# Performance work log

Measured on AMD Instinct MI355X. Metric: run time of the kernel, lower is better.

Reference implementation:

```python
import jax, jax.numpy as jnp
import numpy as np
import math

H, KVH, DH = 8, 1, 256
CAP = 50.0
THETA = 10000.0
HIDDEN = [2048, 1024, 1024]


def _rope_cos_sin(pos, dh=DH, theta=THETA):
    # pos: [b, s] int -> cos/sin: [b, s, dh] (Gemma style: freqs duplicated)
    inv_freq = 1.0 / (theta ** (jnp.arange(0, dh, 2, dtype=jnp.float32) / dh))
    freqs = pos.astype(jnp.float32)[..., None] * inv_freq  # [b, s, dh/2]
    emb = jnp.concatenate([freqs, freqs], axis=-1)
    return jnp.cos(emb), jnp.sin(emb)


def _rotate_half(x):
    x1, x2 = jnp.split(x, 2, axis=-1)
    return jnp.concatenate([-x2, x1], axis=-1)


def _apply_rope(q, k, cos, sin):
    # q: [b,H,s,d], k: [b,KVH,s,d]; cos/sin: [b,s,d] -> broadcast over heads
    c = cos[:, None].astype(q.dtype)
    s = sin[:, None].astype(q.dtype)
    return q * c + _rotate_half(q) * s, k * c + _rotate_half(k) * s


def setup_inputs() -> dict:
    key = jax.random.key(0)
    ks = jax.random.split(key, 32)
    inp = {
        'hs0': jax.random.normal(ks[0], (8, 968, 2048), jnp.float32),
        'hs1': jax.random.normal(ks[1], (8, 6, 1024), jnp.float32),
        'hs2': jax.random.normal(ks[2], (8, 50, 1024), jnp.float32),
        'attention_mask': jnp.zeros((8, 1, 1024, 1024), jnp.float32),
        'pos0': jnp.sort(jax.random.randint(ks[3], (8, 968), 0, 1024), axis=-1),
        'pos1': jnp.sort(jax.random.randint(ks[4], (8, 6), 0, 1024), axis=-1),
        'pos2': jnp.sort(jax.random.randint(ks[5], (8, 50), 0, 1024), axis=-1),
    }
    ki = 6
    for b, hid in enumerate(HIDDEN):
        inp[f'wq{b}'] = 0.02 * jax.random.normal(ks[ki + 0], (hid, H * DH), jnp.float32)
        inp[f'wk{b}'] = 0.02 * jax.random.normal(ks[ki + 1], (hid, KVH * DH), jnp.float32)
        inp[f'wv{b}'] = 0.02 * jax.random.normal(ks[ki + 2], (hid, KVH * DH), jnp.float32)
        inp[f'wo{b}'] = 0.02 * jax.random.normal(ks[ki + 3], (H * DH, hid), jnp.float32)
        ki += 4
    return inp


def _joint_attn(hs_all, pos_all, mask, wq, wk, wv, wo):
    b = hs_all[0].shape[0]
    q_lens = [h.shape[1] for h in hs_all]
    qs, kss, vs = [], [], []
    for hs, pos, Wq, Wk, Wv in zip(hs_all, pos_all, wq, wk, wv):
        s = hs.shape[1]
        q = (hs @ Wq).reshape(b, s, H, DH).transpose(0, 2, 1, 3)
        k = (hs @ Wk).reshape(b, s, KVH, DH).transpose(0, 2, 1, 3)
        v = (hs @ Wv).reshape(b, s, KVH, DH).transpose(0, 2, 1, 3)
        cos, sin = _rope_cos_sin(pos)
        q, k = _apply_rope(q, k, cos, sin)
        # repeat_kv: MQA -> expand KV heads to H
        qs.append(q)
        kss.append(jnp.repeat(k, H // KVH, axis=1))
        vs.append(jnp.repeat(v, H // KVH, axis=1))
    q = jnp.concatenate(qs, axis=2)   # [b,H,S,d]
    k = jnp.concatenate(kss, axis=2)
    v = jnp.concatenate(vs, axis=2)
    scores = jnp.einsum('bhqd,bhkd->bhqk', q, k) / math.sqrt(DH)
    scores = jnp.tanh(scores / CAP) * CAP + mask  # tanh soft-capping
    p = jax.nn.softmax(scores.astype(jnp.float32), axis=-1).astype(q.dtype)
    out = jnp.einsum('bhqk,bhkd->bhqd', p, v)     # [b,H,S,d]
    out = out.transpose(0, 2, 1, 3).reshape(b, sum(q_lens), H * DH)
    outs, off = [], 0
    for ql, Wo in zip(q_lens, wo):
        outs.append(out[:, off:off + ql] @ Wo)
        off += ql
    return tuple(outs)


def reference(hs0, hs1, hs2, attention_mask, pos0, pos1, pos2,
              wq0, wk0, wv0, wo0, wq1, wk1, wv1, wo1, wq2, wk2, wv2, wo2):
    return _joint_attn((hs0, hs1, hs2), (pos0, pos1, pos2), attention_mask,
                       (wq0, wq1, wq2), (wk0, wk1, wk2), (wv0, wv1, wv2),
                       (wo0, wo1, wo2))
```

## Files before the change

kernel.cpp:

```cpp
#include <hip/hip_runtime.h>
#include <hip/hip_bf16.h>
#include <math.h>

namespace {
constexpr int Bn = 8, Sn = 1024, Hn = 8, DHn = 256, HDn = 2048;
constexpr size_t QB0 = 0;
constexpr size_t QB1 = (size_t)20 * 64 * 4096;
constexpr size_t QB2 = QB1 + (size_t)20 * 32 * 4096;
constexpr size_t HB0 = 0;
constexpr size_t HB1 = (size_t)61 * 64 * 4096;
constexpr size_t HB2 = HB1 + (size_t)1 * 32 * 4096;
constexpr size_t OB0 = 0;
constexpr size_t OB1 = (size_t)16 * 64 * 4096;
constexpr size_t OB2 = OB1 + (size_t)8 * 64 * 4096;
}

using bf16x8 = __attribute__((ext_vector_type(8))) short;
using f32x4  = __attribute__((ext_vector_type(4))) float;

__device__ __forceinline__ float bf2f(unsigned short u) {
  unsigned int x = ((unsigned int)u) << 16;
  return __builtin_bit_cast(float, x);
}
__device__ __forceinline__ unsigned short f2bf(float f) {
  unsigned int x = __builtin_bit_cast(unsigned int, f);
  x += 0x7fff + ((x >> 16) & 1);
  return (unsigned short)(x >> 16);
}
__device__ __forceinline__ bf16x8 pack8(const float4& u, const float4& v) {
  bf16x8 r;
  r[0] = (short)f2bf(u.x); r[1] = (short)f2bf(u.y); r[2] = (short)f2bf(u.z); r[3] = (short)f2bf(u.w);
  r[4] = (short)f2bf(v.x); r[5] = (short)f2bf(v.y); r[6] = (short)f2bf(v.z); r[7] = (short)f2bf(v.w);
  return r;
}
__device__ __forceinline__ void gload_lds16(const void* g, void* l) {
  __builtin_amdgcn_global_load_lds(
      (const __attribute__((address_space(1))) void*)g,
      (__attribute__((address_space(3))) void*)l, 16, 0, 0);
}

__device__ __forceinline__ void convW_body(
    const float* __restrict__ W, unsigned short* __restrict__ dstBase,
    int K, int N, int nb, int kb, float (*S)[132], int t)
{
  const int kl = t >> 5, nq = (t & 31) * 4;
  for (int kk = kl; kk < 64; kk += 8) {
    const float4 v = *(const float4*)(W + (size_t)(kb * 64 + kk) * N + nb * 128 + nq);
    S[kk][nq] = v.x; S[kk][nq + 1] = v.y; S[kk][nq + 2] = v.z; S[kk][nq + 3] = v.w;
  }
  __syncthreads();
  unsigned short* chunk = dstBase + ((size_t)nb * (K >> 5) + kb * 2) * 4096;
#pragma unroll
  for (int j = 0; j < 4; ++j) {
    const int q = t * 4 + j;
    const int r = q >> 3, g = q & 7;
    bf16x8 o;
#pragma unroll
    for (int e = 0; e < 8; ++e) o[e] = (short)f2bf(S[g * 8 + e][r]);
    *(bf16x8*)(chunk + (g >> 2) * 4096 + r * 32 + (((g & 3) ^ ((r >> 1) & 3)) * 8)) = o;
  }
}

__global__ __launch_bounds__(256) void convAll(
    const float* __restrict__ wq0, const float* __restrict__ wk0, const float* __restrict__ wv0,
    const float* __restrict__ wq1, const float* __restrict__ wk1, const float* __restrict__ wv1,
    const float* __restrict__ wq2, const float* __restrict__ wk2, const float* __restrict__ wv2,
    const float* __restrict__ hs0, const float* __restrict__ hs1, const float* __restrict__ hs2,
    unsigned short* __restrict__ qkvT, unsigned short* __restrict__ hsT)
{
  __shared__ float S[64][132];
  const int bid = blockIdx.x;
  const int t = threadIdx.x;

  if (bid < 1280) {
    const float* W; unsigned short* dst; int K, N, nb, kb;
    if (bid < 512)       { W = wq0; dst = qkvT + QB0;                  K = 2048; N = 2048; nb = bid & 15; kb = bid >> 4; }
    else if (bid < 576)  { int r = bid - 512;  W = wk0; dst = qkvT + QB0 + (size_t)16 * 64 * 4096; K = 2048; N = 256; nb = r & 1; kb = r >> 1; }
    else if (bid < 640)  { int r = bid - 576;  W = wv0; dst = qkvT + QB0 + (size_t)18 * 64 * 4096; K = 2048; N = 256; nb = r & 1; kb = r >> 1; }
    else if (bid < 896)  { int r = bid - 640;  W = wq1; dst = qkvT + QB1;                  K = 1024; N = 2048; nb = r & 15; kb = r >> 4; }
    else if (bid < 928)  { int r = bid - 896;  W = wk1; dst = qkvT + QB1 + (size_t)16 * 32 * 4096; K = 1024; N = 256; nb = r & 1; kb = r >> 1; }
    else if (bid < 960)  { int r = bid - 928;  W = wv1; dst = qkvT + QB1 + (size_t)18 * 32 * 4096; K = 1024; N = 256; nb = r & 1; kb = r >> 1; }
    else if (bid < 1216) { int r = bid - 960;  W = wq2; dst = qkvT + QB2;                  K = 1024; N = 2048; nb = r & 15; kb = r >> 4; }
    else if (bid < 1248) { int r = bid - 1216; W = wk2; dst = qkvT + QB2 + (size_t)16 * 32 * 4096; K = 1024; N = 256; nb = r & 1; kb = r >> 1; }
    else                 { int r = bid - 1248; W = wv2; dst = qkvT + QB2 + (size_t)18 * 32 * 4096; K = 1024; N = 256; nb = r & 1; kb = r >> 1; }
    convW_body(W, dst, K, N, nb, kb, S, t);
  } else {
    const float* A; unsigned short* dst; int K, M_total, mb, kb;
    if (bid < 3232)      { int it = bid - 1280; A = hs0; dst = hsT + HB0; K = 2048; M_total = 7744; mb = it >> 5; kb = it & 31; }
    else if (bid < 3248) { int it = bid - 3232; A = hs1; dst = hsT + HB1; K = 1024; M_total = 48;   mb = 0;       kb = it; }
    else                 { int it = bid - 3248; A = hs2; dst = hsT + HB2; K = 1024; M_total = 400;  mb = it >> 4; kb = it & 15; }
    unsigned short* chunk = dst + ((size_t)mb * (K >> 5) + kb * 2) * 4096;
#pragma unroll
    for (int j = 0; j < 4; ++j) {
      const int q = j * 256 + t;
      const int r = q >> 3, g = q & 7;
      int m = mb * 128 + r;
      if (m >= M_total) m = mb * 128;
      const float* src = A + (size_t)m * K + kb * 64 + g * 8;
      const float4 u = *(const float4*)(src);
      const float4 v = *(const float4*)(src + 4);
      *(bf16x8*)(chunk + (g >> 2) * 4096 + r * 32 + (((g & 3) ^ ((r >> 1) & 3)) * 8)) = pack8(u, v);
    }
  }
}

__global__ __launch_bounds__(256) void convWo(
    const float* __restrict__ wo0, const float* __restrict__ wo1, const float* __restrict__ wo2,
    unsigned short* __restrict__ woT)
{
  __shared__ float S[64][132];
  const int bid = blockIdx.x;
  const float* W; unsigned short* dst; int N, nb, kb;
  if (bid < 512)      { W = wo0; dst = woT + OB0; N = 2048; nb = bid & 15; kb = bid >> 4; }
  else if (bid < 768) { int r = bid - 512; W = wo1; dst = woT + OB1; N = 1024; nb = r & 7; kb = r >> 3; }
  else                { int r = bid - 768; W = wo2; dst = woT + OB2; N = 1024; nb = r & 7; kb = r >> 3; }
  convW_body(W, dst, HDn, N, nb, kb, S, threadIdx.x);
}

__global__ __launch_bounds__(256) void gemm_qkv(
    const unsigned short* __restrict__ hsT, const unsigned short* __restrict__ qkvT,
    unsigned short* __restrict__ Qh, unsigned short* __restrict__ Kh,
    unsigned short* __restrict__ Vt)
{
  __shared__ __align__(16) short As[2][4096];
  __shared__ __align__(16) short Bs[2][4096];
  const int tid = threadIdx.x;
  const int w  = tid >> 6, l = tid & 63;
  const int wm = w >> 1,  wn = w & 1;
  const int lc = l & 15,  lg = l >> 4;

  const int bid = blockIdx.x;
  int bx, by, L, K, c_off, M_total;
  const unsigned short *aBase, *wBase;
  if (bid < 1220)      { bx = bid % 20; by = bid / 20; L = 968; K = 2048; c_off = 0;   M_total = 7744; aBase = hsT + HB0; wBase = qkvT + QB0; }
  else if (bid < 1240) { bx = bid - 1220; by = 0;      L = 6;   K = 1024; c_off = 968; M_total = 48;   aBase = hsT + HB1; wBase = qkvT + QB1; }
  else                 { int r = bid - 1240; bx = r % 20; by = r / 20; L = 50; K = 1024; c_off = 974; M_total = 400; aBase = hsT + HB2; wBase = qkvT + QB2; }
  const int kcN = K >> 5;
  const int bm0 = by * 128;

  int region, nbL, cb0;
  if (bx < 16)      { region = 0; nbL = bx;      cb0 = bx * 128; }
  else if (bx < 18) { region = 1; nbL = bx - 16; cb0 = (bx - 16) * 128; }
  else              { region = 2; nbL = bx - 18; cb0 = (bx - 18) * 128; }
  const unsigned short* WTr = wBase +
      (region == 0 ? (size_t)0 : (region == 1 ? (size_t)16 * kcN * 4096
                                              : (size_t)18 * kcN * 4096));
  const char* bChunk0 = (const char*)(WTr + (size_t)nbL * kcN * 4096);
  const char* aChunk0 = (const char*)(aBase + (size_t)by * kcN * 4096);

  f32x4 acc[4][4];
#pragma unroll
  for (int i = 0; i < 4; ++i)
#pragma unroll
    for (int j = 0; j < 4; ++j) acc[i][j] = (f32x4){0.f, 0.f, 0.f, 0.f};

  auto issue = [&](int kc, int nb) {
    const char* sa = aChunk0 + (size_t)kc * 8192;
    const char* sb = bChunk0 + (size_t)kc * 8192;
    char* da = (char*)&As[nb][0];
    char* db = (char*)&Bs[nb][0];
    gload_lds16(sa + tid * 16, da + tid * 16);
    gload_lds16(sa + tid * 16 + 4096, da + tid * 16 + 4096);
    gload_lds16(sb + tid * 16, db + tid * 16);
    gload_lds16(sb + tid * 16 + 4096, db + tid * 16 + 4096);
  };

  issue(0, 0);
  for (int kt = 0; kt < kcN; ++kt) {
    const int cur = kt & 1;
    __builtin_amdgcn_s_barrier();
    if (kt + 1 < kcN) {
      issue(kt + 1, cur ^ 1);
      asm volatile("s_waitcnt vmcnt(4)" ::: "memory");
    } else {
      asm volatile("s_waitcnt vmcnt(0)" ::: "memory");
    }
    __builtin_amdgcn_s_barrier();
    __builtin_amdgcn_sched_barrier(0);
    bf16x8 af[4], bfg[4];
#pragma unroll
    for (int mi = 0; mi < 4; ++mi) {
      const int row = wm * 64 + mi * 16 + lc;
      af[mi] = *(const bf16x8*)((const char*)&As[cur][0] + row * 64 +
                                ((lg ^ ((row >> 1) & 3)) * 16));
    }
#pragma unroll
    for (int ni = 0; ni < 4; ++ni) {
      const int row = wn * 64 + ni * 16 + lc;
      bfg[ni] = *(const bf16x8*)((const char*)&Bs[cur][0] + row * 64 +
                                 ((lg ^ ((row >> 1) & 3)) * 16));
    }
#pragma unroll
    for (int mi = 0; mi < 4; ++mi)
#pragma unroll
      for (int ni = 0; ni < 4; ++ni)
        acc[mi][ni] = __builtin_amdgcn_mfma_f32_16x16x32_bf16(af[mi], bfg[ni], acc[mi][ni], 0, 0, 0);
  }

#pragma unroll
  for (int mi = 0; mi < 4; ++mi) {
    const int gm = bm0 + wm * 64 + mi * 16 + lg * 4;
#pragma unroll
    for (int r = 0; r < 4; ++r) {
      const int m = gm + r;
      if (m < M_total) {
        const int cb = m / L, cs = m - cb * L;
#pragma unroll
        for (int ni = 0; ni < 4; ++ni) {
          const int colL = cb0 + wn * 64 + ni * 16 + lc;
          const unsigned short v = f2bf(acc[mi][ni][r]);
          if (region == 0) {
            const int hh = colL >> 8, dd = colL & 255;
            Qh[(((size_t)cb * Hn + hh) * Sn + c_off + cs) * DHn + dd] = v;
          } else if (region == 1) {
            Kh[((size_t)cb * Sn + c_off + cs) * DHn + colL] = v;
          } else {
            Vt[((size_t)cb * DHn + colL) * Sn + c_off + cs] = v;
          }
        }
      }
    }
  }
}

__global__ __launch_bounds__(256) void gemm_wo(
    const unsigned short* __restrict__ A, const unsigned short* __restrict__ woT,
    float* __restrict__ C)
{
  __shared__ __align__(16) short As[2][4096];
  __shared__ __align__(16) short Bs[2][4096];
  const int tid = threadIdx.x;
  const int w  = tid >> 6, l = tid & 63;
  const int wm = w >> 1,  wn = w & 1;
  const int lc = l & 15,  lg = l >> 4;

  const int bid = blockIdx.x;
  int bx, by, L, N, a_off, M_total;
  const unsigned short* wb;
  float* Cg;
  if (bid < 976)      { bx = bid & 15; by = bid >> 4; L = 968; N = 2048; a_off = 0;   M_total = 7744; wb = woT + OB0; Cg = C; }
  else if (bid < 984) { bx = bid - 976; by = 0;       L = 6;   N = 1024; a_off = 968; M_total = 48;   wb = woT + OB1; Cg = C + (size_t)7744 * 2048; }
  else                { int r = bid - 984; bx = r & 7; by = r >> 3; L = 50; N = 1024; a_off = 974; M_total = 400; wb = woT + OB2; Cg = C + (size_t)7744 * 2048 + (size_t)48 * 1024; }
  const int bm0 = by * 128;
  const char* chunk0 = (const char*)(wb + (size_t)bx * 64 * 4096);

  const int gcont = (tid & 3) ^ ((tid >> 3) & 3);
  const char* aRow[2];
#pragma unroll
  for (int j = 0; j < 2; ++j) {
    int m = bm0 + (tid >> 2) + j * 64;
    if (m >= M_total) m = 0;
    const int cb = m / L, cs = m - cb * L;
    aRow[j] = (const char*)(A + (size_t)(cb * Sn + a_off + cs) * HDn) + gcont * 16;
  }

  f32x4 acc[4][4];
#pragma unroll
  for (int i = 0; i < 4; ++i)
#pragma unroll
    for (int j = 0; j < 4; ++j) acc[i][j] = (f32x4){0.f, 0.f, 0.f, 0.f};

  auto issue = [&](int kc, int nb) {
    char* da = (char*)&As[nb][0];
    char* db = (char*)&Bs[nb][0];
    gload_lds16(aRow[0] + (size_t)kc * 64, da + tid * 16);
    gload_lds16(aRow[1] + (size_t)kc * 64, da + tid * 16 + 4096);
    const char* sb = chunk0 + (size_t)kc * 8192;
    gload_lds16(sb + tid * 16, db + tid * 16);
    gload_lds16(sb + tid * 16 + 4096, db + tid * 16 + 4096);
  };

  issue(0, 0);
  for (int kt = 0; kt < 64; ++kt) {
    const int cur = kt & 1;
    __builtin_amdgcn_s_barrier();
    if (kt + 1 < 64) {
      issue(kt + 1, cur ^ 1);
      asm volatile("s_waitcnt vmcnt(4)" ::: "memory");
    } else {
      asm volatile("s_waitcnt vmcnt(0)" ::: "memory");
    }
    __builtin_amdgcn_s_barrier();
    __builtin_amdgcn_sched_barrier(0);
    bf16x8 af[4], bfg[4];
#pragma unroll
    for (int mi = 0; mi < 4; ++mi) {
      const int row = wm * 64 + mi * 16 + lc;
      af[mi] = *(const bf16x8*)((const char*)&As[cur][0] + row * 64 +
                                ((lg ^ ((row >> 1) & 3)) * 16));
    }
#pragma unroll
    for (int ni = 0; ni < 4; ++ni) {
      const int row = wn * 64 + ni * 16 + lc;
      bfg[ni] = *(const bf16x8*)((const char*)&Bs[cur][0] + row * 64 +
                                 ((lg ^ ((row >> 1) & 3)) * 16));
    }
#pragma unroll
    for (int mi = 0; mi < 4; ++mi)
#pragma unroll
      for (int ni = 0; ni < 4; ++ni)
        acc[mi][ni] = __builtin_amdgcn_mfma_f32_16x16x32_bf16(af[mi], bfg[ni], acc[mi][ni], 0, 0, 0);
  }

#pragma unroll
  for (int mi = 0; mi < 4; ++mi) {
    const int gm = bm0 + wm * 64 + mi * 16 + lg * 4;
#pragma unroll
    for (int r = 0; r < 4; ++r) {
      const int m = gm + r;
      if (m < M_total) {
        const int cb = m / L, cs = m - cb * L;
#pragma unroll
        for (int ni = 0; ni < 4; ++ni) {
          const int col = bx * 128 + wn * 64 + ni * 16 + lc;
          Cg[(size_t)(cb * L + cs) * N + col] = acc[mi][ni][r];
        }
      }
    }
  }
}

__global__ __launch_bounds__(128) void rope_k(
    unsigned short* __restrict__ Kh,
    const int* __restrict__ p0, const int* __restrict__ p1, const int* __restrict__ p2)
{
  const int t = blockIdx.x, b = t >> 10, s = t & 1023;
  int p;
  if (s < 968)      p = p0[b * 968 + s];
  else if (s < 974) p = p1[b * 6 + (s - 968)];
  else              p = p2[b * 50 + (s - 974)];
  const float pf = (float)p;
  const float c0 = -0.07195578415606394f;
  const int d = threadIdx.x;
  const float inv = __expf(c0 * (float)d);
  float cs, sn;
  sincosf(pf * inv, &sn, &cs);
  unsigned short* base = Kh + ((size_t)b * Sn + s) * DHn;
  const float x1 = bf2f(base[d]), x2 = bf2f(base[d + 128]);
  base[d]       = f2bf(x1 * cs - x2 * sn);
  base[d + 128] = f2bf(x2 * cs + x1 * sn);
}

__global__ __launch_bounds__(512) void attn_mfma(
    const unsigned short* __restrict__ Qh, const unsigned short* __restrict__ Kh,
    const unsigned short* __restrict__ Vt, const float* __restrict__ mask,
    const int* __restrict__ p0, const int* __restrict__ p1, const int* __restrict__ p2,
    unsigned short* __restrict__ O)
{
  __shared__ __align__(16) short KsB[2][8192];
  __shared__ __align__(16) short VsB[2][8192];
  __shared__ __align__(16) float Ms[2][512];
  __shared__ __align__(16) short Pb[8][512];
  const int tid = threadIdx.x;
  const int w  = tid >> 6;
  const int l  = tid & 63;
  const int lc = l & 15;
  const int lg = l >> 4;
  const int q0 = blockIdx.x * 16;
  const int b  = blockIdx.z;
  const int srow = q0 + lc;

  const char* KgB = (const char*)(Kh + (size_t)b * Sn * DHn);
  const char* VgB = (const char*)(Vt + (size_t)b * DHn * Sn);

  auto stage = [&](int kt, int nb) {
    const char* kg = KgB + (size_t)kt * 16384;
    const char* vg = VgB + (size_t)kt * 64;
#pragma unroll
    for (int j = 0; j < 2; ++j) {
      const int chunk = w * 2 + j;
      const int o = chunk * 1024 + l * 16;
      const int srcK = o ^ (((o >> 9) & 7) << 4);
      gload_lds16(kg + srcK, (char*)&KsB[nb][0] + chunk * 1024);
    }
#pragma unroll
    for (int j = 0; j < 2; ++j) {
      const int chunk = w * 2 + j;
      const int o = chunk * 1024 + l * 16;
      const int x = o ^ (((o >> 7) & 3) << 4);
      gload_lds16(vg + (size_t)(x >> 6) * 2048 + (x & 63),
                  (char*)&VsB[nb][0] + chunk * 1024);
    }
    if (l < 16) {
      const float* mg = mask + ((size_t)b * Sn + q0 + 2 * w + (l >> 3)) * Sn
                             + kt * 32 + (l & 7) * 4;
      gload_lds16(mg, (char*)&Ms[nb][0] + w * 256);
    }
  };

  stage(0, 0);

  int p;
  if (srow < 968)      p = p0[b * 968 + srow];
  else if (srow < 974) p = p1[b * 6 + (srow - 968)];
  else                 p = p2[b * 50 + (srow - 974)];
  const float pf = (float)p;
  const float c0 = -0.07195578415606394f;

  const unsigned short* qrow = Qh + (((size_t)b * Hn + w) * Sn + srow) * DHn;
  bf16x8 qf[8];
#pragma unroll
  for (int dt = 0; dt < 8; ++dt)
    qf[dt] = *(const bf16x8*)(qrow + dt * 32 + lg * 8);
#pragma unroll
  for (int dt = 0; dt < 4; ++dt) {
#pragma unroll
    for (int j = 0; j < 8; ++j) {
      const int d = dt * 32 + lg * 8 + j;
      const float inv = __expf(c0 * (float)d);
      float cs, sn;
      sincosf(pf * inv, &sn, &cs);
      const float x1 = bf2f((unsigned short)qf[dt][j]);
      const float x2 = bf2f((unsigned short)qf[dt + 4][j]);
      qf[dt][j]     = (short)f2bf(x1 * cs - x2 * sn);
      qf[dt + 4][j] = (short)f2bf(x2 * cs + x1 * sn);
    }
  }

  f32x4 accO[16];
#pragma unroll
  for (int i = 0; i < 16; ++i) accO[i] = (f32x4){0.f, 0.f, 0.f, 0.f};
  float lsum[4] = {0.f, 0.f, 0.f, 0.f};

  const float C1 = 3.6067376022e-3f;
  const float RC = -144.26950408889634f;
  const float L2E = 1.4426950408889634f;

  int cur = 0;
  for (int kt = 0; kt < 32; ++kt) {
    if (kt + 1 < 32) {
      stage(kt + 1, cur ^ 1);
      asm volatile("s_waitcnt vmcnt(5)" ::: "memory");
    } else {
      asm volatile("s_waitcnt vmcnt(0)" ::: "memory");
    }
    __builtin_amdgcn_s_barrier();
    __builtin_amdgcn_sched_barrier(0);

    const short* Ks = &KsB[cur][0];
    const short* Vs = &VsB[cur][0];
    const float* Mw = &Ms[cur][0];

    f32x4 sc[2];
    __builtin_amdgcn_s_setprio(1);
#pragma unroll
    for (int ct = 0; ct < 2; ++ct) {
      f32x4 acc = (f32x4){0.f, 0.f, 0.f, 0.f};
      const int row = ct * 16 + lc;
      const int sw = (row & 7) << 4;
#pragma unroll
      for (int dt = 0; dt < 8; ++dt) {
        const int byt = (row * 512 + dt * 64 + lg * 16) ^ sw;
        const bf16x8 kf = *(const bf16x8*)((const char*)Ks + byt);
        acc = __builtin_amdgcn_mfma_f32_16x16x32_bf16(qf[dt], kf, acc, 0, 0, 0);
      }
      sc[ct] = acc;
    }
    __builtin_amdgcn_s_setprio(0);

#pragma unroll
    for (int ct = 0; ct < 2; ++ct) {
#pragma unroll
      for (int r = 0; r < 4; ++r) {
        const int row_p = lg * 4 + r;
        const float mv = Mw[row_p * 32 + ct * 16 + lc];
        const float e2 = __builtin_amdgcn_exp2f(sc[ct][r] * C1);
        const float rr = __builtin_amdgcn_rcpf(e2 + 1.f);
        const float pv = __builtin_amdgcn_exp2f(fmaf(rr, RC, mv * L2E));
        lsum[r] += pv;
        const int col = ct * 16 + lc;
        const int gp = (col >> 3) ^ ((row_p >> 1) & 3);
        *((short*)((char*)&Pb[w][0] + row_p * 64 + gp * 16 + (col & 7) * 2)) =
            (short)f2bf(pv);
      }
    }
    const int gp2 = lg ^ ((lc >> 1) & 3);
    const bf16x8 pfr = *(const bf16x8*)((const char*)&Pb[w][0] + lc * 64 + gp2 * 16);

    __builtin_amdgcn_s_setprio(1);
#pragma unroll
    for (int nt = 0; nt < 16; ++nt) {
      const int row = nt * 16 + lc;
      const int byt = (row * 64 + lg * 16) ^ (((row >> 1) & 3) << 4);
      const bf16x8 vf = *(const bf16x8*)((const char*)Vs + byt);
      accO[nt] = __builtin_amdgcn_mfma_f32_16x16x32_bf16(pfr, vf, accO[nt], 0, 0, 0);
    }
    __builtin_amdgcn_s_setprio(0);

    __builtin_amdgcn_s_barrier();
    cur ^= 1;
  }

#pragma unroll
  for (int mm = 1; mm < 16; mm <<= 1) {
#pragma unroll
    for (int r = 0; r < 4; ++r) lsum[r] += __shfl_xor(lsum[r], mm);
  }
  float rinv[4];
#pragma unroll
  for (int r = 0; r < 4; ++r) rinv[r] = 1.f / lsum[r];

  unsigned short* obase = O + ((size_t)b * Sn + q0 + lg * 4) * HDn + w * DHn + lc;
#pragma unroll
  for (int nt = 0; nt < 16; ++nt)
#pragma unroll
    for (int r = 0; r < 4; ++r)
      obase[(size_t)r * HDn + nt * 16] = f2bf(accO[nt][r] * rinv[r]);
}

extern "C" void kernel_launch(void* const* d_in, const int* in_sizes, int n_in,
                              void* d_out, int out_size, void* d_ws, size_t ws_size,
                              hipStream_t stream) {
  (void)in_sizes; (void)n_in; (void)out_size; (void)ws_size;
  const float* hs0  = (const float*)d_in[0];
  const float* hs1  = (const float*)d_in[1];
  const float* hs2  = (const float*)d_in[2];
  const float* mask = (const float*)d_in[3];
  const int*   pos0 = (const int*)d_in[4];
  const int*   pos1 = (const int*)d_in[5];
  const int*   pos2 = (const int*)d_in[6];
  float* out = (float*)d_out;

  unsigned short* Qh = (unsigned short*)d_ws;
  unsigned short* Kh = Qh + (size_t)Bn * Sn * HDn;
  unsigned short* Vt = Kh + (size_t)Bn * Sn * DHn;
  unsigned short* Ob = Vt + (size_t)Bn * Sn * DHn;
  unsigned short* qkvT = Ob;
  unsigned short* woT  = Qh;
  unsigned short* hsT  = (unsigned short*)out;

  hipLaunchKernelGGL(convAll, dim3(3312), dim3(256), 0, stream,
                     (const float*)d_in[7],  (const float*)d_in[8],  (const float*)d_in[9],
                     (const float*)d_in[11], (const float*)d_in[12], (const float*)d_in[13],
                     (const float*)d_in[15], (const float*)d_in[16], (const float*)d_in[17],
                     hs0, hs1, hs2, qkvT, hsT);

  hipLaunchKernelGGL(gemm_qkv, dim3(1320), dim3(256), 0, stream,
                     hsT, qkvT, Qh, Kh, Vt);

  hipLaunchKernelGGL(rope_k, dim3(Bn * Sn), dim3(128), 0, stream, Kh, pos0, pos1, pos2);
  hipLaunchKernelGGL(attn_mfma, dim3(Sn / 16, 1, Bn), dim3(512), 0, stream,
                     Qh, Kh, Vt, mask, pos0, pos1, pos2, Ob);

  hipLaunchKernelGGL(convWo, dim3(1024), dim3(256), 0, stream,
                     (const float*)d_in[10], (const float*)d_in[14], (const float*)d_in[18], woT);

  hipLaunchKernelGGL(gemm_wo, dim3(1016), dim3(256), 0, stream, Ob, woT, out);
}
```

Before: 424.7 us.

## Process two heads per wave in attention to reuse K/V fragment loads

```diff
diff --git a/kernel.cpp b/kernel.cpp
--- a/kernel.cpp
+++ b/kernel.cpp
@@ -341,7 +341,7 @@
   base[d + 128] = f2bf(x2 * cs + x1 * sn);
 }
 
-__global__ __launch_bounds__(512) void attn_mfma(
+__global__ __launch_bounds__(256) void attn_mfma(
     const unsigned short* __restrict__ Qh, const unsigned short* __restrict__ Kh,
     const unsigned short* __restrict__ Vt, const float* __restrict__ mask,
     const int* __restrict__ p0, const int* __restrict__ p1, const int* __restrict__ p2,
@@ -350,7 +350,7 @@
   __shared__ __align__(16) short KsB[2][8192];
   __shared__ __align__(16) short VsB[2][8192];
   __shared__ __align__(16) float Ms[2][512];
-  __shared__ __align__(16) short Pb[8][512];
+  __shared__ __align__(16) short Pb[4][1024];
   const int tid = threadIdx.x;
   const int w  = tid >> 6;
   const int l  = tid & 63;
@@ -367,24 +367,24 @@
     const char* kg = KgB + (size_t)kt * 16384;
     const char* vg = VgB + (size_t)kt * 64;
 #pragma unroll
-    for (int j = 0; j < 2; ++j) {
-      const int chunk = w * 2 + j;
+    for (int j = 0; j < 4; ++j) {
+      const int chunk = w * 4 + j;
       const int o = chunk * 1024 + l * 16;
       const int srcK = o ^ (((o >> 9) & 7) << 4);
       gload_lds16(kg + srcK, (char*)&KsB[nb][0] + chunk * 1024);
     }
 #pragma unroll
-    for (int j = 0; j < 2; ++j) {
-      const int chunk = w * 2 + j;
+    for (int j = 0; j < 4; ++j) {
+      const int chunk = w * 4 + j;
       const int o = chunk * 1024 + l * 16;
       const int x = o ^ (((o >> 7) & 3) << 4);
       gload_lds16(vg + (size_t)(x >> 6) * 2048 + (x & 63),
                   (char*)&VsB[nb][0] + chunk * 1024);
     }
-    if (l < 16) {
-      const float* mg = mask + ((size_t)b * Sn + q0 + 2 * w + (l >> 3)) * Sn
+    if (l < 32) {
+      const float* mg = mask + ((size_t)b * Sn + q0 + 4 * w + (l >> 3)) * Sn
                              + kt * 32 + (l & 7) * 4;
-      gload_lds16(mg, (char*)&Ms[nb][0] + w * 256);
+      gload_lds16(mg, (char*)&Ms[nb][0] + w * 512);
     }
   };
 
@@ -397,11 +397,14 @@
   const float pf = (float)p;
   const float c0 = -0.07195578415606394f;
 
-  const unsigned short* qrow = Qh + (((size_t)b * Hn + w) * Sn + srow) * DHn;
-  bf16x8 qf[8];
-#pragma unroll
-  for (int dt = 0; dt < 8; ++dt)
-    qf[dt] = *(const bf16x8*)(qrow + dt * 32 + lg * 8);
+  const unsigned short* qrowA = Qh + (((size_t)b * Hn + 2 * w) * Sn + srow) * DHn;
+  const unsigned short* qrowB = Qh + (((size_t)b * Hn + 2 * w + 1) * Sn + srow) * DHn;
+  bf16x8 qfA[8], qfB[8];
+#pragma unroll
+  for (int dt = 0; dt < 8; ++dt) {
+    qfA[dt] = *(const bf16x8*)(qrowA + dt * 32 + lg * 8);
+    qfB[dt] = *(const bf16x8*)(qrowB + dt * 32 + lg * 8);
+  }
 #pragma unroll
   for (int dt = 0; dt < 4; ++dt) {
 #pragma unroll
@@ -410,17 +413,29 @@
       const float inv = __expf(c0 * (float)d);
       float cs, sn;
       sincosf(pf * inv, &sn, &cs);
-      const float x1 = bf2f((unsigned short)qf[dt][j]);
-      const float x2 = bf2f((unsigned short)qf[dt + 4][j]);
-      qf[dt][j]     = (short)f2bf(x1 * cs - x2 * sn);
-      qf[dt + 4][j] = (short)f2bf(x2 * cs + x1 * sn);
-    }
-  }
-
-  f32x4 accO[16];
-#pragma unroll
-  for (int i = 0; i < 16; ++i) accO[i] = (f32x4){0.f, 0.f, 0.f, 0.f};
-  float lsum[4] = {0.f, 0.f, 0.f, 0.f};
+      {
+        const float x1 = bf2f((unsigned short)qfA[dt][j]);
+        const float x2 = bf2f((unsigned short)qfA[dt + 4][j]);
+        qfA[dt][j]     = (short)f2bf(x1 * cs - x2 * sn);
+        qfA[dt + 4][j] = (short)f2bf(x2 * cs + x1 * sn);
+      }
+      {
+        const float x1 = bf2f((unsigned short)qfB[dt][j]);
+        const float x2 = bf2f((unsigned short)qfB[dt + 4][j]);
+        qfB[dt][j]     = (short)f2bf(x1 * cs - x2 * sn);
+        qfB[dt + 4][j] = (short)f2bf(x2 * cs + x1 * sn);
+      }
+    }
+  }
+
+  f32x4 accA[16], accB[16];
+#pragma unroll
+  for (int i = 0; i < 16; ++i) {
+    accA[i] = (f32x4){0.f, 0.f, 0.f, 0.f};
+    accB[i] = (f32x4){0.f, 0.f, 0.f, 0.f};
+  }
+  float lsumA[4] = {0.f, 0.f, 0.f, 0.f};
+  float lsumB[4] = {0.f, 0.f, 0.f, 0.f};
 
   const float C1 = 3.6067376022e-3f;
   const float RC = -144.26950408889634f;
@@ -430,7 +445,7 @@
   for (int kt = 0; kt < 32; ++kt) {
     if (kt + 1 < 32) {
       stage(kt + 1, cur ^ 1);
-      asm volatile("s_waitcnt vmcnt(5)" ::: "memory");
+      asm volatile("s_waitcnt vmcnt(9)" ::: "memory");
     } else {
       asm volatile("s_waitcnt vmcnt(0)" ::: "memory");
     }
@@ -441,20 +456,22 @@
     const short* Vs = &VsB[cur][0];
     const float* Mw = &Ms[cur][0];
 
-    f32x4 sc[2];
+    f32x4 scA[2], scB[2];
     __builtin_amdgcn_s_setprio(1);
 #pragma unroll
     for (int ct = 0; ct < 2; ++ct) {
-      f32x4 acc = (f32x4){0.f, 0.f, 0.f, 0.f};
+      f32x4 aA = (f32x4){0.f, 0.f, 0.f, 0.f};
+      f32x4 aB = (f32x4){0.f, 0.f, 0.f, 0.f};
       const int row = ct * 16 + lc;
       const int sw = (row & 7) << 4;
 #pragma unroll
       for (int dt = 0; dt < 8; ++dt) {
         const int byt = (row * 512 + dt * 64 + lg * 16) ^ sw;
         const bf16x8 kf = *(const bf16x8*)((const char*)Ks + byt);
-        acc = __builtin_amdgcn_mfma_f32_16x16x32_bf16(qf[dt], kf, acc, 0, 0, 0);
+        aA = __builtin_amdgcn_mfma_f32_16x16x32_bf16(qfA[dt], kf, aA, 0, 0, 0);
+        aB = __builtin_amdgcn_mfma_f32_16x16x32_bf16(qfB[dt], kf, aB, 0, 0, 0);
       }
-      sc[ct] = acc;
+      scA[ct] = aA; scB[ct] = aB;
     }
     __builtin_amdgcn_s_setprio(0);
 
@@ -463,19 +480,29 @@
 #pragma unroll
       for (int r = 0; r < 4; ++r) {
         const int row_p = lg * 4 + r;
-        const float mv = Mw[row_p * 32 + ct * 16 + lc];
-        const float e2 = __builtin_amdgcn_exp2f(sc[ct][r] * C1);
-        const float rr = __builtin_amdgcn_rcpf(e2 + 1.f);
-        const float pv = __builtin_amdgcn_exp2f(fmaf(rr, RC, mv * L2E));
-        lsum[r] += pv;
         const int col = ct * 16 + lc;
+        const float mvl = Mw[row_p * 32 + col] * L2E;
         const int gp = (col >> 3) ^ ((row_p >> 1) & 3);
-        *((short*)((char*)&Pb[w][0] + row_p * 64 + gp * 16 + (col & 7) * 2)) =
-            (short)f2bf(pv);
+        const int pbyt = row_p * 64 + gp * 16 + (col & 7) * 2;
+        {
+          const float e2 = __builtin_amdgcn_exp2f(scA[ct][r] * C1);
+          const float rr = __builtin_amdgcn_rcpf(e2 + 1.f);
+          const float pv = __builtin_amdgcn_exp2f(fmaf(rr, RC, mvl));
+          lsumA[r] += pv;
+          *((short*)((char*)&Pb[w][0] + pbyt)) = (short)f2bf(pv);
+        }
+        {
+          const float e2 = __builtin_amdgcn_exp2f(scB[ct][r] * C1);
+          const float rr = __builtin_amdgcn_rcpf(e2 + 1.f);
+          const float pv = __builtin_amdgcn_exp2f(fmaf(rr, RC, mvl));
+          lsumB[r] += pv;
+          *((short*)((char*)&Pb[w][0] + 1024 + pbyt)) = (short)f2bf(pv);
+        }
       }
     }
     const int gp2 = lg ^ ((lc >> 1) & 3);
-    const bf16x8 pfr = *(const bf16x8*)((const char*)&Pb[w][0] + lc * 64 + gp2 * 16);
+    const bf16x8 pfA = *(const bf16x8*)((const char*)&Pb[w][0] + lc * 64 + gp2 * 16);
+    const bf16x8 pfB = *(const bf16x8*)((const char*)&Pb[w][0] + 1024 + lc * 64 + gp2 * 16);
 
     __builtin_amdgcn_s_setprio(1);
 #pragma unroll
@@ -483,7 +510,8 @@
       const int row = nt * 16 + lc;
       const int byt = (row * 64 + lg * 16) ^ (((row >> 1) & 3) << 4);
       const bf16x8 vf = *(const bf16x8*)((const char*)Vs + byt);
-      accO[nt] = __builtin_amdgcn_mfma_f32_16x16x32_bf16(pfr, vf, accO[nt], 0, 0, 0);
+      accA[nt] = __builtin_amdgcn_mfma_f32_16x16x32_bf16(pfA, vf, accA[nt], 0, 0, 0);
+      accB[nt] = __builtin_amdgcn_mfma_f32_16x16x32_bf16(pfB, vf, accB[nt], 0, 0, 0);
     }
     __builtin_amdgcn_s_setprio(0);
 
@@ -494,18 +522,27 @@
 #pragma unroll
   for (int mm = 1; mm < 16; mm <<= 1) {
 #pragma unroll
-    for (int r = 0; r < 4; ++r) lsum[r] += __shfl_xor(lsum[r], mm);
-  }
-  float rinv[4];
-#pragma unroll
-  for (int r = 0; r < 4; ++r) rinv[r] = 1.f / lsum[r];
-
-  unsigned short* obase = O + ((size_t)b * Sn + q0 + lg * 4) * HDn + w * DHn + lc;
+    for (int r = 0; r < 4; ++r) {
+      lsumA[r] += __shfl_xor(lsumA[r], mm);
+      lsumB[r] += __shfl_xor(lsumB[r], mm);
+    }
+  }
+  float rinvA[4], rinvB[4];
+#pragma unroll
+  for (int r = 0; r < 4; ++r) {
+    rinvA[r] = 1.f / lsumA[r];
+    rinvB[r] = 1.f / lsumB[r];
+  }
+
+  unsigned short* obA = O + ((size_t)b * Sn + q0 + lg * 4) * HDn + (2 * w) * DHn + lc;
+  unsigned short* obB = obA + DHn;
 #pragma unroll
   for (int nt = 0; nt < 16; ++nt)
 #pragma unroll
-    for (int r = 0; r < 4; ++r)
-      obase[(size_t)r * HDn + nt * 16] = f2bf(accO[nt][r] * rinv[r]);
+    for (int r = 0; r < 4; ++r) {
+      obA[(size_t)r * HDn + nt * 16] = f2bf(accA[nt][r] * rinvA[r]);
+      obB[(size_t)r * HDn + nt * 16] = f2bf(accB[nt][r] * rinvB[r]);
+    }
 }
 
 extern "C" void kernel_launch(void* const* d_in, const int* in_sizes, int n_in,
@@ -539,7 +576,7 @@
                      hsT, qkvT, Qh, Kh, Vt);
 
   hipLaunchKernelGGL(rope_k, dim3(Bn * Sn), dim3(128), 0, stream, Kh, pos0, pos1, pos2);
-  hipLaunchKernelGGL(attn_mfma, dim3(Sn / 16, 1, Bn), dim3(512), 0, stream,
+  hipLaunchKernelGGL(attn_mfma, dim3(Sn / 16, 1, Bn), dim3(256), 0, stream,
                      Qh, Kh, Vt, mask, pos0, pos1, pos2, Ob);
 
   hipLaunchKernelGGL(convWo, dim3(1024), dim3(256), 0, stream,
```

Result: slower. 473.8 us (+11.6%).

## Compute transposed scores and redistribute P via bpermute instead of LDS

Applied to the files above, without the earlier changes.

```diff
diff --git a/kernel.cpp b/kernel.cpp
--- a/kernel.cpp
+++ b/kernel.cpp
@@ -17,6 +17,7 @@
 
 using bf16x8 = __attribute__((ext_vector_type(8))) short;
 using f32x4  = __attribute__((ext_vector_type(4))) float;
+using i32x4  = __attribute__((ext_vector_type(4))) int;
 
 __device__ __forceinline__ float bf2f(unsigned short u) {
   unsigned int x = ((unsigned int)u) << 16;
@@ -37,6 +38,11 @@
   __builtin_amdgcn_global_load_lds(
       (const __attribute__((address_space(1))) void*)g,
       (__attribute__((address_space(3))) void*)l, 16, 0, 0);
+}
+__device__ __forceinline__ unsigned cvtpk(float lo, float hi) {
+  unsigned r;
+  asm("v_cvt_pk_bf16_f32 %0, %1, %2" : "=v"(r) : "v"(lo), "v"(hi));
+  return r;
 }
 
 __device__ __forceinline__ void convW_body(
@@ -341,7 +347,7 @@
   base[d + 128] = f2bf(x2 * cs + x1 * sn);
 }
 
-__global__ __launch_bounds__(512) void attn_mfma(
+__global__ __launch_bounds__(512, 4) void attn_mfma(
     const unsigned short* __restrict__ Qh, const unsigned short* __restrict__ Kh,
     const unsigned short* __restrict__ Vt, const float* __restrict__ mask,
     const int* __restrict__ p0, const int* __restrict__ p1, const int* __restrict__ p2,
@@ -350,7 +356,6 @@
   __shared__ __align__(16) short KsB[2][8192];
   __shared__ __align__(16) short VsB[2][8192];
   __shared__ __align__(16) float Ms[2][512];
-  __shared__ __align__(16) short Pb[8][512];
   const int tid = threadIdx.x;
   const int w  = tid >> 6;
   const int l  = tid & 63;
@@ -382,8 +387,9 @@
                   (char*)&VsB[nb][0] + chunk * 1024);
     }
     if (l < 16) {
-      const float* mg = mask + ((size_t)b * Sn + q0 + 2 * w + (l >> 3)) * Sn
-                             + kt * 32 + (l & 7) * 4;
+      const int q = 2 * w + (l >> 3);
+      const int kb = (((l & 7) * 4) - 4 * q) & 31;
+      const float* mg = mask + ((size_t)b * Sn + q0 + q) * Sn + kt * 32 + kb;
       gload_lds16(mg, (char*)&Ms[nb][0] + w * 256);
     }
   };
@@ -420,11 +426,17 @@
   f32x4 accO[16];
 #pragma unroll
   for (int i = 0; i < 16; ++i) accO[i] = (f32x4){0.f, 0.f, 0.f, 0.f};
-  float lsum[4] = {0.f, 0.f, 0.f, 0.f};
+  float lsum = 0.f;
 
   const float C1 = 3.6067376022e-3f;
   const float RC = -144.26950408889634f;
   const float L2E = 1.4426950408889634f;
+
+  const int mo0 = lc * 128 + (((lg * 4) + 4 * lc) & 31) * 4;
+  const int mo1 = lc * 128 + (((16 + lg * 4) + 4 * lc) & 31) * 4;
+  const int sidx0 = (((lg & 1) * 2) * 16 + lc) * 4;
+  const int sidx1 = sidx0 + 64;
+  const bool hiT = (lg >= 2);
 
   int cur = 0;
   for (int kt = 0; kt < 32; ++kt) {
@@ -437,9 +449,12 @@
     __builtin_amdgcn_s_barrier();
     __builtin_amdgcn_sched_barrier(0);
 
-    const short* Ks = &KsB[cur][0];
-    const short* Vs = &VsB[cur][0];
-    const float* Mw = &Ms[cur][0];
+    const char* Ks = (const char*)&KsB[cur][0];
+    const char* Vs = (const char*)&VsB[cur][0];
+    const char* Mw = (const char*)&Ms[cur][0];
+
+    const float4 mv0 = *(const float4*)(Mw + mo0);
+    const float4 mv1 = *(const float4*)(Mw + mo1);
 
     f32x4 sc[2];
     __builtin_amdgcn_s_setprio(1);
@@ -451,38 +466,52 @@
 #pragma unroll
       for (int dt = 0; dt < 8; ++dt) {
         const int byt = (row * 512 + dt * 64 + lg * 16) ^ sw;
-        const bf16x8 kf = *(const bf16x8*)((const char*)Ks + byt);
-        acc = __builtin_amdgcn_mfma_f32_16x16x32_bf16(qf[dt], kf, acc, 0, 0, 0);
+        const bf16x8 kf = *(const bf16x8*)(Ks + byt);
+        acc = __builtin_amdgcn_mfma_f32_16x16x32_bf16(kf, qf[dt], acc, 0, 0, 0);
       }
       sc[ct] = acc;
     }
     __builtin_amdgcn_s_setprio(0);
 
-#pragma unroll
-    for (int ct = 0; ct < 2; ++ct) {
+    const float mA[8] = {mv0.x, mv0.y, mv0.z, mv0.w, mv1.x, mv1.y, mv1.z, mv1.w};
+    float pr[8];
+#pragma unroll
+    for (int t = 0; t < 2; ++t) {
 #pragma unroll
       for (int r = 0; r < 4; ++r) {
-        const int row_p = lg * 4 + r;
-        const float mv = Mw[row_p * 32 + ct * 16 + lc];
-        const float e2 = __builtin_amdgcn_exp2f(sc[ct][r] * C1);
+        const float e2 = __builtin_amdgcn_exp2f(sc[t][r] * C1);
         const float rr = __builtin_amdgcn_rcpf(e2 + 1.f);
-        const float pv = __builtin_amdgcn_exp2f(fmaf(rr, RC, mv * L2E));
-        lsum[r] += pv;
-        const int col = ct * 16 + lc;
-        const int gp = (col >> 3) ^ ((row_p >> 1) & 3);
-        *((short*)((char*)&Pb[w][0] + row_p * 64 + gp * 16 + (col & 7) * 2)) =
-            (short)f2bf(pv);
+        const float pv = __builtin_amdgcn_exp2f(fmaf(rr, RC, mA[t * 4 + r] * L2E));
+        lsum += pv;
+        pr[t * 4 + r] = pv;
       }
     }
-    const int gp2 = lg ^ ((lc >> 1) & 3);
-    const bf16x8 pfr = *(const bf16x8*)((const char*)&Pb[w][0] + lc * 64 + gp2 * 16);
+
+    const int t0w0 = (int)cvtpk(pr[0], pr[1]);
+    const int t0w1 = (int)cvtpk(pr[2], pr[3]);
+    const int t1w0 = (int)cvtpk(pr[4], pr[5]);
+    const int t1w1 = (int)cvtpk(pr[6], pr[7]);
+    const int b00 = __builtin_amdgcn_ds_bpermute(sidx0, t0w0);
+    const int b01 = __builtin_amdgcn_ds_bpermute(sidx0, t0w1);
+    const int b02 = __builtin_amdgcn_ds_bpermute(sidx1, t0w0);
+    const int b03 = __builtin_amdgcn_ds_bpermute(sidx1, t0w1);
+    const int b10 = __builtin_amdgcn_ds_bpermute(sidx0, t1w0);
+    const int b11 = __builtin_amdgcn_ds_bpermute(sidx0, t1w1);
+    const int b12 = __builtin_amdgcn_ds_bpermute(sidx1, t1w0);
+    const int b13 = __builtin_amdgcn_ds_bpermute(sidx1, t1w1);
+    i32x4 pd;
+    pd[0] = hiT ? b10 : b00;
+    pd[1] = hiT ? b11 : b01;
+    pd[2] = hiT ? b12 : b02;
+    pd[3] = hiT ? b13 : b03;
+    const bf16x8 pfr = __builtin_bit_cast(bf16x8, pd);
 
     __builtin_amdgcn_s_setprio(1);
 #pragma unroll
     for (int nt = 0; nt < 16; ++nt) {
       const int row = nt * 16 + lc;
       const int byt = (row * 64 + lg * 16) ^ (((row >> 1) & 3) << 4);
-      const bf16x8 vf = *(const bf16x8*)((const char*)Vs + byt);
+      const bf16x8 vf = *(const bf16x8*)(Vs + byt);
       accO[nt] = __builtin_amdgcn_mfma_f32_16x16x32_bf16(pfr, vf, accO[nt], 0, 0, 0);
     }
     __builtin_amdgcn_s_setprio(0);
@@ -491,21 +520,19 @@
     cur ^= 1;
   }
 
-#pragma unroll
-  for (int mm = 1; mm < 16; mm <<= 1) {
-#pragma unroll
-    for (int r = 0; r < 4; ++r) lsum[r] += __shfl_xor(lsum[r], mm);
-  }
-  float rinv[4];
-#pragma unroll
-  for (int r = 0; r < 4; ++r) rinv[r] = 1.f / lsum[r];
+  lsum += __shfl_xor(lsum, 16);
+  lsum += __shfl_xor(lsum, 32);
+  const float rinvF = 1.f / lsum;
+  float rv[4];
+#pragma unroll
+  for (int r = 0; r < 4; ++r) rv[r] = __shfl(rinvF, lg * 4 + r);
 
   unsigned short* obase = O + ((size_t)b * Sn + q0 + lg * 4) * HDn + w * DHn + lc;
 #pragma unroll
   for (int nt = 0; nt < 16; ++nt)
 #pragma unroll
     for (int r = 0; r < 4; ++r)
-      obase[(size_t)r * HDn + nt * 16] = f2bf(accO[nt][r] * rinv[r]);
+      obase[(size_t)r * HDn + nt * 16] = f2bf(accO[nt][r] * rv[r]);
 }
 
 extern "C" void kernel_launch(void* const* d_in, const int* in_sizes, int n_in,
```

Result: slower. 821.6 us (+93.4%).
